# Optimization experiments

Hardware: AMD Instinct MI355X
Metric: run time of the kernel (lower is better)

## Reference

```python
import jax, jax.numpy as jnp
import numpy as np

NEG_SLOPE = 0.2


def gat_conv(x, src, dst, W, att_src, att_dst, bias, heads, out_ch):
    # x: [N, Fin]; src/dst: [E] (self-loops already included)
    N = x.shape[0]
    h = (x @ W).reshape(N, heads, out_ch)                      # [N, H, C]
    a_s = jnp.einsum('nhc,hc->nh', h, att_src)                 # [N, H]
    a_d = jnp.einsum('nhc,hc->nh', h, att_dst)                 # [N, H]
    e = jax.nn.leaky_relu(a_s[src] + a_d[dst], NEG_SLOPE)      # [E, H]
    # segment softmax over incoming edges of each dst node
    e_max = jax.ops.segment_max(e, dst, num_segments=N)        # [N, H]
    p = jnp.exp(e - e_max[dst])                                # [E, H]
    denom = jax.ops.segment_sum(p, dst, num_segments=N)        # [N, H]
    alpha = p / denom[dst]                                     # [E, H]
    msg = h[src] * alpha[:, :, None]                           # [E, H, C]
    out = jax.ops.segment_sum(msg, dst, num_segments=N)        # [N, H, C]
    return out.reshape(N, heads * out_ch) + bias


def setup_inputs() -> dict:
    key = jax.random.key(0)
    ks = jax.random.split(key, 10)
    N, E, F_IN, HID, HEADS, NCLS = 100000, 3200000, 512, 8, 8, 16
    x = jax.random.normal(ks[0], (N, F_IN), dtype=jnp.float32)
    edge_index = jax.random.randint(ks[1], (2, E), 0, N, dtype=jnp.int64)
    s = 1.0 / np.sqrt(F_IN)
    W1 = jax.random.uniform(ks[2], (F_IN, HEADS * HID), jnp.float32, -s, s)
    att_src1 = jax.random.normal(ks[3], (HEADS, HID), jnp.float32) * 0.1
    att_dst1 = jax.random.normal(ks[4], (HEADS, HID), jnp.float32) * 0.1
    b1 = jnp.zeros((HEADS * HID,), jnp.float32)
    s2 = 1.0 / np.sqrt(HEADS * HID)
    W2 = jax.random.uniform(ks[5], (HEADS * HID, NCLS), jnp.float32, -s2, s2)
    att_src2 = jax.random.normal(ks[6], (1, NCLS), jnp.float32) * 0.1
    att_dst2 = jax.random.normal(ks[7], (1, NCLS), jnp.float32) * 0.1
    b2 = jnp.zeros((NCLS,), jnp.float32)
    return {"x": x, "edge_index": edge_index, "W1": W1, "att_src1": att_src1,
            "att_dst1": att_dst1, "b1": b1, "W2": W2, "att_src2": att_src2,
            "att_dst2": att_dst2, "b2": b2}


def reference(x, edge_index, W1, att_src1, att_dst1, b1, W2, att_src2, att_dst2, b2):
    N = x.shape[0]
    loops = jnp.arange(N, dtype=edge_index.dtype)
    src = jnp.concatenate([edge_index[0], loops])  # PyG add_self_loops=True
    dst = jnp.concatenate([edge_index[1], loops])
    # eval mode: F.dropout is identity
    h = gat_conv(x, src, dst, W1, att_src1, att_dst1, b1, heads=8, out_ch=8)
    h = jax.nn.elu(h)
    out = gat_conv(h, src, dst, W2, att_src2, att_dst2, b2, heads=1, out_ch=16)
    return out
```

## Files before the change

### kernel.cpp

```cpp
#include <hip/hip_runtime.h>

#define F_IN 512
#define F1 64
#define NCLS 16
#define NEG_SLOPE 0.2f

typedef __attribute__((ext_vector_type(8))) short short8;
typedef __attribute__((ext_vector_type(4))) float f32x4;

__device__ __forceinline__ unsigned short f2bf(float f) {
    unsigned u = __float_as_uint(f);
    return (unsigned short)((u + 0x7fffu + ((u >> 16) & 1u)) >> 16);
}
__device__ __forceinline__ float bf2f(unsigned short u) {
    return __uint_as_float(((unsigned)u) << 16);
}


__global__ __launch_bounds__(64) void k_detect(const int* __restrict__ ei, int E,
                                               unsigned* __restrict__ mode) {
    int t = threadIdx.x;
    unsigned nz = 0;
    int lim = (E > 256) ? 256 : E;
    for (int k = t; k < lim; k += 64) nz |= (unsigned)ei[2 * k + 1];
    for (int off = 1; off < 64; off <<= 1) nz |= __shfl_xor(nz, off);
    if (t == 0) *mode = (nz == 0) ? 1u : 0u;
}

__device__ __forceinline__ void decode_edge(const int* __restrict__ ei,
                                            const long long* __restrict__ e64,
                                            bool m64, unsigned i, int E, int N,
                                            int& s, int& v) {
    if (i < (unsigned)E) {
        if (m64) { s = (int)e64[i]; v = (int)e64[E + i]; }
        else     { s = ei[i];       v = ei[E + i]; }
    } else {
        s = (int)(i - (unsigned)E);
        v = s;
    }
    s = s < 0 ? 0 : (s >= N ? N - 1 : s);
    v = v < 0 ? 0 : (v >= N ? N - 1 : v);
}

__device__ __forceinline__ int decode_dst(const int* __restrict__ ei,
                                          const long long* __restrict__ e64,
                                          bool m64, unsigned i, int E, int N) {
    int v;
    if (i < (unsigned)E) v = m64 ? (int)e64[E + i] : ei[E + i];
    else                 v = (int)(i - (unsigned)E);
    return v < 0 ? 0 : (v >= N ? N - 1 : v);
}


__global__ __launch_bounds__(256) void k_prep(const float* __restrict__ W1,
                                              unsigned short* __restrict__ W1T) {
    int t = blockIdx.x * 256 + threadIdx.x;
    if (t < F_IN * F1) {
        int k = t >> 6, c = t & 63;
        W1T[(size_t)c * F_IN + k] = f2bf(W1[t]);
    }
}


__device__ __forceinline__ void gemm1_tile(const float* __restrict__ x,
                                           const unsigned short* __restrict__ W1T,
                                           const float* __restrict__ att_s,
                                           const float* __restrict__ att_d,
                                           unsigned short* __restrict__ h1b,
                                           float* __restrict__ a_s1,
                                           float* __restrict__ a_d1,
                                           int N, int row0,
                                           unsigned short (*Abuf)[40],
                                           unsigned short (*BbufT)[40]) {
    const int tid = threadIdx.x;
    const int w = tid >> 6, lane = tid & 63;
    const int quad = lane >> 4, r16 = lane & 15;

    f32x4 acc[4];
#pragma unroll
    for (int t = 0; t < 4; t++) acc[t] = (f32x4){0.f, 0.f, 0.f, 0.f};

    const int a_row = tid >> 2;
    const int a_seg = (tid & 3) * 8;
    const int b_col = tid & 63;
    const int b_kq  = tid >> 6;
    const int ar = row0 + a_row;

    for (int k0 = 0; k0 < F_IN; k0 += 32) {
        {
            float4 v0 = make_float4(0.f, 0.f, 0.f, 0.f), v1 = v0;
            if (ar < N) {
                const float* xp = x + (size_t)ar * F_IN + k0 + a_seg;
                v0 = *(const float4*)xp;
                v1 = *(const float4*)(xp + 4);
            }
            short8 cv;
            cv[0] = (short)f2bf(v0.x); cv[1] = (short)f2bf(v0.y);
            cv[2] = (short)f2bf(v0.z); cv[3] = (short)f2bf(v0.w);
            cv[4] = (short)f2bf(v1.x); cv[5] = (short)f2bf(v1.y);
            cv[6] = (short)f2bf(v1.z); cv[7] = (short)f2bf(v1.w);
            *(short8*)&Abuf[a_row][a_seg] = cv;
        }
        {
            const unsigned short* wp = W1T + (size_t)b_col * F_IN + k0 + b_kq * 8;
            *(short8*)&BbufT[b_col][b_kq * 8] = *(const short8*)wp;
        }
        __syncthreads();

        short8 af = *(const short8*)&Abuf[w * 16 + r16][quad * 8];
#pragma unroll
        for (int t = 0; t < 4; t++) {
            short8 bf = *(const short8*)&BbufT[t * 16 + r16][quad * 8];
            acc[t] = __builtin_amdgcn_mfma_f32_16x16x32_bf16(af, bf, acc[t], 0, 0, 0);
        }
        __syncthreads();
    }

    float ats[4], atd[4];
#pragma unroll
    for (int t = 0; t < 4; t++) {
        ats[t] = att_s[t * 16 + r16];
        atd[t] = att_d[t * 16 + r16];
    }
#pragma unroll
    for (int r = 0; r < 4; r++) {
        int grow = row0 + w * 16 + quad * 4 + r;
        bool ok = grow < N;
        float ps[4], pd[4];
#pragma unroll
        for (int t = 0; t < 4; t++) {
            float vv = acc[t][r];
            if (ok) h1b[(size_t)grow * F1 + t * 16 + r16] = f2bf(vv);
            ps[t] = vv * ats[t];
            pd[t] = vv * atd[t];
        }
#pragma unroll
        for (int t = 0; t < 4; t++) {
            ps[t] += __shfl_xor(ps[t], 1); pd[t] += __shfl_xor(pd[t], 1);
            ps[t] += __shfl_xor(ps[t], 2); pd[t] += __shfl_xor(pd[t], 2);
            ps[t] += __shfl_xor(ps[t], 4); pd[t] += __shfl_xor(pd[t], 4);
        }
        if (ok && (r16 & 7) == 0) {
            int hh0 = r16 >> 3;
#pragma unroll
            for (int t = 0; t < 4; t++) {
                a_s1[(size_t)grow * 8 + t * 2 + hh0] = ps[t];
                a_d1[(size_t)grow * 8 + t * 2 + hh0] = pd[t];
            }
        }
    }
}


__global__ __launch_bounds__(256) void k_fusedA(const float* __restrict__ x,
                                                const unsigned short* __restrict__ W1T,
                                                const float* __restrict__ att_s,
                                                const float* __restrict__ att_d,
                                                unsigned short* __restrict__ h1b,
                                                float* __restrict__ a_s1,
                                                float* __restrict__ a_d1, int N,
                                                const int* __restrict__ ei,
                                                const unsigned* __restrict__ mode,
                                                unsigned* __restrict__ bucketCnt,
                                                int E, int ET, int nch,
                                                int nb, int shift) {
    __shared__ __align__(16) char smem[10240];
    unsigned b = blockIdx.x;
    if ((b & 1) == 0) {
        gemm1_tile(x, W1T, att_s, att_d, h1b, a_s1, a_d1, N, (int)(b >> 1) * 64,
                   (unsigned short (*)[40])smem,
                   (unsigned short (*)[40])(smem + 5120));
        return;
    }
    unsigned* cntL = (unsigned*)smem;
    for (int i = threadIdx.x; i < 1024; i += 256) cntL[i] = 0u;
    __syncthreads();

    const unsigned stride = (unsigned)nch * 256u;
    bool m64 = (*mode != 0u);
    const long long* e64 = (const long long*)ei;
    unsigned i = (b >> 1) * 256u + threadIdx.x;
    for (; i + 3u * stride < (unsigned)ET; i += 4u * stride) {
        int v0 = decode_dst(ei, e64, m64, i, E, N);
        int v1 = decode_dst(ei, e64, m64, i + stride, E, N);
        int v2 = decode_dst(ei, e64, m64, i + 2u * stride, E, N);
        int v3 = decode_dst(ei, e64, m64, i + 3u * stride, E, N);
        atomicAdd(&cntL[(unsigned)v0 >> shift], 1u);
        atomicAdd(&cntL[(unsigned)v1 >> shift], 1u);
        atomicAdd(&cntL[(unsigned)v2 >> shift], 1u);
        atomicAdd(&cntL[(unsigned)v3 >> shift], 1u);
    }
    for (; i < (unsigned)ET; i += stride) {
        int v = decode_dst(ei, e64, m64, i, E, N);
        atomicAdd(&cntL[(unsigned)v >> shift], 1u);
    }
    __syncthreads();
    for (int k = threadIdx.x; k < nb; k += 256) {
        unsigned c = cntL[k];
        if (c) atomicAdd(&bucketCnt[k], c);
    }
}


__global__ __launch_bounds__(256) void k_fusedB(const float* __restrict__ x,
                                                const unsigned short* __restrict__ W1T,
                                                const float* __restrict__ att_s,
                                                const float* __restrict__ att_d,
                                                unsigned short* __restrict__ h1b,
                                                float* __restrict__ a_s1,
                                                float* __restrict__ a_d1, int N,
                                                int rowSplit,
                                                const int* __restrict__ ei,
                                                const unsigned* __restrict__ mode,
                                                unsigned* __restrict__ bucketFill,
                                                unsigned* __restrict__ pairs,
                                                int E, int ET, int nch,
                                                int nb, int shift) {
    __shared__ __align__(16) char smem[10240];
    unsigned b = blockIdx.x;
    if (b & 1) {
        gemm1_tile(x, W1T, att_s, att_d, h1b, a_s1, a_d1, N,
                   rowSplit + (int)(b >> 1) * 64,
                   (unsigned short (*)[40])smem,
                   (unsigned short (*)[40])(smem + 5120));
        return;
    }
    unsigned* cntA = (unsigned*)smem;
    unsigned* ofsA = (unsigned*)(smem + 4096);
    unsigned* part = (unsigned*)(smem + 8192);
    const int t = threadIdx.x;
    const int chunk = (ET + nch - 1) / nch;
    const int cbase = (int)(b >> 1) * chunk;
    const int cend = (cbase + chunk < ET) ? cbase + chunk : ET;
    const unsigned lmask = (1u << shift) - 1u;
    bool m64 = (*mode != 0u);
    const long long* e64 = (const long long*)ei;

    for (int k = t; k < 1024; k += 256) cntA[k] = 0u;
    __syncthreads();
    for (int k = cbase + t; k < cend; k += 256) {
        int v = decode_dst(ei, e64, m64, (unsigned)k, E, N);
        atomicAdd(&cntA[(unsigned)v >> shift], 1u);
    }
    __syncthreads();
    unsigned a0 = cntA[4 * t + 0], a1 = cntA[4 * t + 1];
    unsigned a2 = cntA[4 * t + 2], a3 = cntA[4 * t + 3];
    unsigned ssum = a0 + a1 + a2 + a3;
    part[t] = ssum;
    __syncthreads();
    for (int off = 1; off < 256; off <<= 1) {
        unsigned add = (t >= off) ? part[t - off] : 0u;
        __syncthreads();
        part[t] += add;
        __syncthreads();
    }
    unsigned excl = part[t] - ssum;
    ofsA[4 * t + 0] = excl;
    ofsA[4 * t + 1] = excl + a0;
    ofsA[4 * t + 2] = excl + a0 + a1;
    ofsA[4 * t + 3] = excl + a0 + a1 + a2;
    __syncthreads();
    for (int k = t; k < nb; k += 256) {
        unsigned c = cntA[k];
        unsigned g = c ? atomicAdd(&bucketFill[k], c) : 0u;
        cntA[k] = g - ofsA[k];
    }
    __syncthreads();
    for (int k = cbase + t; k < cend; k += 256) {
        int s, v;
        decode_edge(ei, e64, m64, (unsigned)k, E, N, s, v);
        unsigned bb = (unsigned)v >> shift;
        unsigned slot = atomicAdd(&ofsA[bb], 1u);
        pairs[cntA[bb] + slot] = (unsigned)s | (((unsigned)v & lmask) << 20);
    }
}


__global__ __launch_bounds__(1024) void k_scan_buckets(const unsigned* __restrict__ bucketCnt,
                                                       int nb, int ET,
                                                       unsigned* __restrict__ bucketOfs,
                                                       unsigned* __restrict__ bucketFill,
                                                       unsigned* __restrict__ row_ptr,
                                                       int N) {
    __shared__ unsigned sbuf[1024];
    int t = threadIdx.x;
    unsigned val = (t < nb) ? bucketCnt[t] : 0u;
    sbuf[t] = val;
    __syncthreads();
    for (int off = 1; off < 1024; off <<= 1) {
        unsigned add = (t >= off) ? sbuf[t - off] : 0u;
        __syncthreads();
        sbuf[t] += add;
        __syncthreads();
    }
    if (t < nb) {
        unsigned e = sbuf[t] - val;
        bucketOfs[t] = e;
        bucketFill[t] = e;
    }
    if (t == 0) row_ptr[N] = (unsigned)ET;
}


__global__ __launch_bounds__(256) void k_sort(const unsigned* __restrict__ pairs,
                                              const unsigned* __restrict__ bucketOfs,
                                              const unsigned* __restrict__ bucketCnt,
                                              unsigned* __restrict__ row_ptr,
                                              unsigned* __restrict__ ssrc,
                                              int N, int shift) {
    __shared__ unsigned f[1024];
    __shared__ unsigned part[256];
    const int b = blockIdx.x;
    const int t = threadIdx.x;
    const int nodes = 1 << shift;
    const int bbase = b << shift;
    for (int i = t; i < 1024; i += 256) f[i] = 0u;
    __syncthreads();
    const unsigned base = bucketOfs[b];
    const unsigned cnt = bucketCnt[b];
    for (unsigned i = (unsigned)t; i < cnt; i += 256u)
        atomicAdd(&f[pairs[base + i] >> 20], 1u);
    __syncthreads();
    unsigned a0 = f[4 * t + 0], a1 = f[4 * t + 1];
    unsigned a2 = f[4 * t + 2], a3 = f[4 * t + 3];
    unsigned ssum = a0 + a1 + a2 + a3;
    part[t] = ssum;
    __syncthreads();
    for (int off = 1; off < 256; off <<= 1) {
        unsigned add = (t >= off) ? part[t - off] : 0u;
        __syncthreads();
        part[t] += add;
        __syncthreads();
    }
    unsigned excl = part[t] - ssum;
    unsigned c0 = base + excl;
    unsigned c1 = c0 + a0;
    unsigned c2 = c1 + a1;
    unsigned c3 = c2 + a2;
    {
        int v0 = bbase + 4 * t;
        if (v0 + 0 < N && 4 * t + 0 < nodes) row_ptr[v0 + 0] = c0;
        if (v0 + 1 < N && 4 * t + 1 < nodes) row_ptr[v0 + 1] = c1;
        if (v0 + 2 < N && 4 * t + 2 < nodes) row_ptr[v0 + 2] = c2;
        if (v0 + 3 < N && 4 * t + 3 < nodes) row_ptr[v0 + 3] = c3;
    }
    f[4 * t + 0] = c0;
    f[4 * t + 1] = c1;
    f[4 * t + 2] = c2;
    f[4 * t + 3] = c3;
    __syncthreads();
    for (unsigned i = (unsigned)t; i < cnt; i += 256u) {
        unsigned pk = pairs[base + i];
        unsigned local = pk >> 20;
        unsigned pos = atomicAdd(&f[local], 1u);
        ssrc[pos] = pk & 0xFFFFFu;
    }
}


__global__ __launch_bounds__(256) void k_agg1(const unsigned short* __restrict__ h1b,
                                              const float* __restrict__ a_s1,
                                              const float* __restrict__ a_d1,
                                              const float* __restrict__ b1,
                                              const unsigned* __restrict__ row_ptr,
                                              const unsigned* __restrict__ ssrc,
                                              float* __restrict__ g, int N) {
    int wid = threadIdx.x >> 6, lane = threadIdx.x & 63;
    int v = blockIdx.x * 4 + wid;
    if (v >= N) return;
    unsigned base = row_ptr[v];
    unsigned deg = row_ptr[v + 1] - base;

    const int eA = lane >> 3, hA = lane & 7;
    float adv = a_d1[(size_t)v * 8 + hA];
    const int half = lane >> 5, j32 = lane & 31;
    const int hq = j32 >> 2;

    float denom = 0.f, acc0 = 0.f, acc1 = 0.f;
    for (unsigned jj = 0; jj < deg; jj += 8) {
        unsigned ee = jj + (unsigned)eA;
        bool val = ee < deg;
        unsigned sL = ssrc[base + (val ? ee : 0u)];
        float as = a_s1[(size_t)sL * 8 + hA];
        float eatt = as + adv;
        eatt = eatt > 0.f ? eatt : NEG_SLOPE * eatt;
        float p = val ? __expf(eatt) : 0.f;
        denom += p;
#pragma unroll
        for (int k = 0; k < 4; k++) {
            int esel = k * 2 + half;
            unsigned s_my = (unsigned)__shfl((int)sL, esel * 8);
            float p_my = __shfl(p, esel * 8 + hq);
            unsigned u = *(const unsigned*)(h1b + ((size_t)s_my << 6) + (j32 << 1));
            float lo = __uint_as_float(u << 16);
            float hi = __uint_as_float(u & 0xffff0000u);
            acc0 = fmaf(lo, p_my, acc0);
            acc1 = fmaf(hi, p_my, acc1);
        }
    }
    acc0 += __shfl_xor(acc0, 32);
    acc1 += __shfl_xor(acc1, 32);
    denom += __shfl_xor(denom, 8);
    denom += __shfl_xor(denom, 16);
    denom += __shfl_xor(denom, 32);
    float dn = __shfl(denom, hq);
    if (half == 0) {
        float inv = 1.0f / dn;
        int c0 = j32 * 2;
        float t0 = acc0 * inv + b1[c0];
        float t1 = acc1 * inv + b1[c0 + 1];
        t0 = t0 > 0.f ? t0 : (__expf(t0) - 1.f);
        t1 = t1 > 0.f ? t1 : (__expf(t1) - 1.f);
        *(float2*)&g[(size_t)v * F1 + c0] = make_float2(t0, t1);
    }
}


__global__ __launch_bounds__(256) void k_gemm2(const float* __restrict__ g,
                                               const float* __restrict__ W2,
                                               const float* __restrict__ as2w,
                                               const float* __restrict__ ad2w,
                                               float* __restrict__ h2,
                                               float* __restrict__ a_s2,
                                               float* __restrict__ a_d2, int N) {
    __shared__ float W2s[F1][NCLS];
    int tid = threadIdx.x;
    for (int i = tid; i < F1 * NCLS; i += 256) ((float*)W2s)[i] = W2[i];
    __syncthreads();
    int lane = tid & 63, wid = tid >> 6;
    int n = blockIdx.x * 16 + wid * 4 + (lane >> 4);
    int c = lane & 15;
    if (n >= N) return;
    float acc = 0.f;
#pragma unroll
    for (int k4 = 0; k4 < 16; k4++) {
        float4 gv = *(const float4*)(g + (size_t)n * F1 + k4 * 4);
        acc = fmaf(gv.x, W2s[k4 * 4 + 0][c], acc);
        acc = fmaf(gv.y, W2s[k4 * 4 + 1][c], acc);
        acc = fmaf(gv.z, W2s[k4 * 4 + 2][c], acc);
        acc = fmaf(gv.w, W2s[k4 * 4 + 3][c], acc);
    }
    h2[(size_t)n * NCLS + c] = acc;
    float s = acc * as2w[c];
    float d = acc * ad2w[c];
    s += __shfl_xor(s, 1); s += __shfl_xor(s, 2); s += __shfl_xor(s, 4); s += __shfl_xor(s, 8);
    d += __shfl_xor(d, 1); d += __shfl_xor(d, 2); d += __shfl_xor(d, 4); d += __shfl_xor(d, 8);
    if (c == 0) { a_s2[n] = s; a_d2[n] = d; }
}


__global__ __launch_bounds__(256) void k_agg2(const float* __restrict__ h2,
                                              const float* __restrict__ a_s2,
                                              const float* __restrict__ a_d2,
                                              const float* __restrict__ b2,
                                              const unsigned* __restrict__ row_ptr,
                                              const unsigned* __restrict__ ssrc,
                                              float* __restrict__ out, int N) {
    int wid = threadIdx.x >> 6, lane = threadIdx.x & 63;
    int v = blockIdx.x * 4 + wid;
    if (v >= N) return;
    unsigned base = row_ptr[v];
    unsigned deg = row_ptr[v + 1] - base;
    float adv = a_d2[v];
    int sub = lane >> 4, c = lane & 15;

    float denom = 0.f, acc = 0.f;
    unsigned j = sub;
    for (; j + 12 < deg; j += 16) {
        unsigned s0 = ssrc[base + j + 0];
        unsigned s1 = ssrc[base + j + 4];
        unsigned s2 = ssrc[base + j + 8];
        unsigned s3 = ssrc[base + j + 12];
        float as0 = a_s2[s0];
        float as1 = a_s2[s1];
        float as2 = a_s2[s2];
        float as3 = a_s2[s3];
        float h0 = h2[(size_t)s0 * NCLS + c];
        float h1v = h2[(size_t)s1 * NCLS + c];
        float h2v = h2[(size_t)s2 * NCLS + c];
        float h3 = h2[(size_t)s3 * NCLS + c];
        float e0 = as0 + adv; e0 = e0 > 0.f ? e0 : NEG_SLOPE * e0; float p0 = __expf(e0);
        float e1 = as1 + adv; e1 = e1 > 0.f ? e1 : NEG_SLOPE * e1; float p1 = __expf(e1);
        float e2 = as2 + adv; e2 = e2 > 0.f ? e2 : NEG_SLOPE * e2; float p2 = __expf(e2);
        float e3 = as3 + adv; e3 = e3 > 0.f ? e3 : NEG_SLOPE * e3; float p3 = __expf(e3);
        denom += (p0 + p1) + (p2 + p3);
        acc = fmaf(h0, p0, acc);
        acc = fmaf(h1v, p1, acc);
        acc = fmaf(h2v, p2, acc);
        acc = fmaf(h3, p3, acc);
    }
    for (; j < deg; j += 4) {
        unsigned s = ssrc[base + j];
        float as = a_s2[s];
        float hv = h2[(size_t)s * NCLS + c];
        float e = as + adv; e = e > 0.f ? e : NEG_SLOPE * e;
        float p = __expf(e);
        denom += p;
        acc = fmaf(hv, p, acc);
    }
    acc += __shfl_xor(acc, 16);
    acc += __shfl_xor(acc, 32);
    denom += __shfl_xor(denom, 16);
    denom += __shfl_xor(denom, 32);
    if (lane < 16) {
        out[(size_t)v * NCLS + c] = acc * (1.0f / denom) + b2[c];
    }
}


static inline size_t algn(size_t x) { return (x + 255) & ~(size_t)255; }

extern "C" void kernel_launch(void* const* d_in, const int* in_sizes, int n_in,
                              void* d_out, int out_size, void* d_ws, size_t ws_size,
                              hipStream_t stream) {
    const float* x   = (const float*)d_in[0];
    const int* ei    = (const int*)d_in[1];
    const float* W1  = (const float*)d_in[2];
    const float* as1 = (const float*)d_in[3];
    const float* ad1 = (const float*)d_in[4];
    const float* b1  = (const float*)d_in[5];
    const float* W2  = (const float*)d_in[6];
    const float* as2 = (const float*)d_in[7];
    const float* ad2 = (const float*)d_in[8];
    const float* b2  = (const float*)d_in[9];

    const int N = in_sizes[0] / F_IN;
    const int E = in_sizes[1] / 2;
    const int ET = E + N;

    int shift = 8;
    int nb = (N + 255) >> 8;
    while (nb > 1024) { shift++; nb = (N + (1 << shift) - 1) >> shift; }

    const int GA_T = ((N / 2) + 63) / 64;
    const int rowSplit = GA_T * 64;
    const int GB_T = (N - rowSplit + 63) / 64;

    char* p = (char*)d_ws;
    unsigned short* h1b = (unsigned short*)p;  p += algn((size_t)N * F1 * 2);
    float* g    = (float*)p;      p += algn((size_t)N * F1 * 4);
    float* a_s1 = (float*)p;      p += algn((size_t)N * 8 * 4);
    float* a_d1 = (float*)p;      p += algn((size_t)N * 8 * 4);
    float* h2   = (float*)p;      p += algn((size_t)N * NCLS * 4);
    float* a_s2 = (float*)p;      p += algn((size_t)N * 4);
    float* a_d2 = (float*)p;      p += algn((size_t)N * 4);
    unsigned* row_ptr = (unsigned*)p;  p += algn((size_t)(N + 1) * 4);
    unsigned* bucketCnt  = (unsigned*)p;  p += algn((size_t)1024 * 4);
    unsigned* bucketOfs  = (unsigned*)p;  p += algn((size_t)1024 * 4);
    unsigned* bucketFill = (unsigned*)p;  p += algn((size_t)1024 * 4);
    unsigned* mode    = (unsigned*)p;  p += algn(256);
    unsigned short* W1T = (unsigned short*)p;  p += algn((size_t)F_IN * F1 * 2);
    unsigned* ssrc = (unsigned*)p;     p += algn((size_t)ET * 4);
    unsigned* pairs = (unsigned*)g;

    hipMemsetAsync(bucketCnt, 0, (size_t)nb * 4, stream);

    dim3 b256(256);
    k_detect<<<dim3(1), dim3(64), 0, stream>>>(ei, E, mode);
    k_prep<<<dim3((F_IN * F1 + 255) / 256), b256, 0, stream>>>(W1, W1T);

    k_fusedA<<<dim3(2 * GA_T), b256, 0, stream>>>(x, W1T, as1, ad1, h1b, a_s1, a_d1, N,
                                                  ei, mode, bucketCnt,
                                                  E, ET, GA_T, nb, shift);

    k_scan_buckets<<<dim3(1), dim3(1024), 0, stream>>>(bucketCnt, nb, ET, bucketOfs,
                                                       bucketFill, row_ptr, N);

    k_fusedB<<<dim3(2 * GB_T), b256, 0, stream>>>(x, W1T, as1, ad1, h1b, a_s1, a_d1, N,
                                                  rowSplit, ei, mode, bucketFill,
                                                  pairs, E, ET, GB_T, nb, shift);

    k_sort<<<dim3(nb), b256, 0, stream>>>(pairs, bucketOfs, bucketCnt, row_ptr, ssrc, N, shift);

    k_agg1<<<dim3((N + 3) / 4), b256, 0, stream>>>(h1b, a_s1, a_d1, b1, row_ptr, ssrc, g, N);
    k_gemm2<<<dim3((N + 15) / 16), b256, 0, stream>>>(g, W2, as2, ad2, h2, a_s2, a_d2, N);
    k_agg2<<<dim3((N + 3) / 4), b256, 0, stream>>>(h2, a_s2, a_d2, b2, row_ptr, ssrc,
                                                   (float*)d_out, N);
}
```

Measured before the change: 631.7 us.

## Double-buffer GEMM1 LDS tiles and store gathered a_s1/h2 in fp16

The layer-1 GEMM tile loop now prefetches the next K-slice of x and W1T into registers while MFMAs run on the current LDS buffer. It alternates between two LDS buffers, so each iteration needs one barrier instead of two. Separately, the per-node source attention scores a_s1 and the layer-2 features h2 are stored as fp16, which halves the bytes gathered per edge in the aggregation kernels. The cost is double the shared memory in the fused kernels, which can lower occupancy, plus some precision loss in the attention logits and layer-2 features.

```diff
diff --git a/kernel.cpp b/kernel.cpp
--- a/kernel.cpp
+++ b/kernel.cpp
@@ -1,4 +1,5 @@
 #include <hip/hip_runtime.h>
+#include <hip/hip_fp16.h>
 
 #define F_IN 512
 #define F1 64
@@ -67,11 +68,9 @@
                                            const float* __restrict__ att_s,
                                            const float* __restrict__ att_d,
                                            unsigned short* __restrict__ h1b,
-                                           float* __restrict__ a_s1,
+                                           __half* __restrict__ a_s1,
                                            float* __restrict__ a_d1,
-                                           int N, int row0,
-                                           unsigned short (*Abuf)[40],
-                                           unsigned short (*BbufT)[40]) {
+                                           int N, int row0, char* sm) {
     const int tid = threadIdx.x;
     const int w = tid >> 6, lane = tid & 63;
     const int quad = lane >> 4, r16 = lane & 15;
@@ -85,35 +84,61 @@
     const int b_col = tid & 63;
     const int b_kq  = tid >> 6;
     const int ar = row0 + a_row;
-
-    for (int k0 = 0; k0 < F_IN; k0 += 32) {
+    const bool arok = ar < N;
+    const float* xrow = x + (size_t)ar * F_IN + a_seg;
+    const unsigned short* wrow = W1T + (size_t)b_col * F_IN + b_kq * 8;
+
+    float4 v0 = make_float4(0.f, 0.f, 0.f, 0.f), v1 = v0;
+    short8 rb;
+    if (arok) { v0 = *(const float4*)(xrow); v1 = *(const float4*)(xrow + 4); }
+    rb = *(const short8*)(wrow);
+    {
+        unsigned short (*A)[40] = (unsigned short (*)[40])(sm);
+        unsigned short (*B)[40] = (unsigned short (*)[40])(sm + 5120);
+        short8 cv;
+        cv[0] = (short)f2bf(v0.x); cv[1] = (short)f2bf(v0.y);
+        cv[2] = (short)f2bf(v0.z); cv[3] = (short)f2bf(v0.w);
+        cv[4] = (short)f2bf(v1.x); cv[5] = (short)f2bf(v1.y);
+        cv[6] = (short)f2bf(v1.z); cv[7] = (short)f2bf(v1.w);
+        *(short8*)&A[a_row][a_seg] = cv;
+        *(short8*)&B[b_col][b_kq * 8] = rb;
+    }
+    __syncthreads();
+
+    int cur = 0;
+#pragma unroll
+    for (int k = 0; k < F_IN / 32; k++) {
+        if (k + 1 < F_IN / 32) {
+            v0 = make_float4(0.f, 0.f, 0.f, 0.f); v1 = v0;
+            if (arok) {
+                const float* xp = xrow + (k + 1) * 32;
+                v0 = *(const float4*)xp; v1 = *(const float4*)(xp + 4);
+            }
+            rb = *(const short8*)(wrow + (k + 1) * 32);
+        }
         {
-            float4 v0 = make_float4(0.f, 0.f, 0.f, 0.f), v1 = v0;
-            if (ar < N) {
-                const float* xp = x + (size_t)ar * F_IN + k0 + a_seg;
-                v0 = *(const float4*)xp;
-                v1 = *(const float4*)(xp + 4);
+            unsigned short (*A)[40] = (unsigned short (*)[40])(sm + cur * 10240);
+            unsigned short (*B)[40] = (unsigned short (*)[40])(sm + cur * 10240 + 5120);
+            short8 af = *(const short8*)&A[w * 16 + r16][quad * 8];
+#pragma unroll
+            for (int t = 0; t < 4; t++) {
+                short8 bf = *(const short8*)&B[t * 16 + r16][quad * 8];
+                acc[t] = __builtin_amdgcn_mfma_f32_16x16x32_bf16(af, bf, acc[t], 0, 0, 0);
             }
+        }
+        if (k + 1 < F_IN / 32) {
+            unsigned short (*A)[40] = (unsigned short (*)[40])(sm + (cur ^ 1) * 10240);
+            unsigned short (*B)[40] = (unsigned short (*)[40])(sm + (cur ^ 1) * 10240 + 5120);
             short8 cv;
             cv[0] = (short)f2bf(v0.x); cv[1] = (short)f2bf(v0.y);
             cv[2] = (short)f2bf(v0.z); cv[3] = (short)f2bf(v0.w);
             cv[4] = (short)f2bf(v1.x); cv[5] = (short)f2bf(v1.y);
             cv[6] = (short)f2bf(v1.z); cv[7] = (short)f2bf(v1.w);
-            *(short8*)&Abuf[a_row][a_seg] = cv;
-        }
-        {
-            const unsigned short* wp = W1T + (size_t)b_col * F_IN + k0 + b_kq * 8;
-            *(short8*)&BbufT[b_col][b_kq * 8] = *(const short8*)wp;
+            *(short8*)&A[a_row][a_seg] = cv;
+            *(short8*)&B[b_col][b_kq * 8] = rb;
         }
         __syncthreads();
-
-        short8 af = *(const short8*)&Abuf[w * 16 + r16][quad * 8];
-#pragma unroll
-        for (int t = 0; t < 4; t++) {
-            short8 bf = *(const short8*)&BbufT[t * 16 + r16][quad * 8];
-            acc[t] = __builtin_amdgcn_mfma_f32_16x16x32_bf16(af, bf, acc[t], 0, 0, 0);
-        }
-        __syncthreads();
+        cur ^= 1;
     }
 
     float ats[4], atd[4];
@@ -144,7 +169,7 @@
             int hh0 = r16 >> 3;
 #pragma unroll
             for (int t = 0; t < 4; t++) {
-                a_s1[(size_t)grow * 8 + t * 2 + hh0] = ps[t];
+                a_s1[(size_t)grow * 8 + t * 2 + hh0] = __float2half_rn(ps[t]);
                 a_d1[(size_t)grow * 8 + t * 2 + hh0] = pd[t];
             }
         }
@@ -157,19 +182,17 @@
                                                 const float* __restrict__ att_s,
                                                 const float* __restrict__ att_d,
                                                 unsigned short* __restrict__ h1b,
-                                                float* __restrict__ a_s1,
+                                                __half* __restrict__ a_s1,
                                                 float* __restrict__ a_d1, int N,
                                                 const int* __restrict__ ei,
                                                 const unsigned* __restrict__ mode,
                                                 unsigned* __restrict__ bucketCnt,
                                                 int E, int ET, int nch,
                                                 int nb, int shift) {
-    __shared__ __align__(16) char smem[10240];
+    __shared__ __align__(16) char smem[20480];
     unsigned b = blockIdx.x;
     if ((b & 1) == 0) {
-        gemm1_tile(x, W1T, att_s, att_d, h1b, a_s1, a_d1, N, (int)(b >> 1) * 64,
-                   (unsigned short (*)[40])smem,
-                   (unsigned short (*)[40])(smem + 5120));
+        gemm1_tile(x, W1T, att_s, att_d, h1b, a_s1, a_d1, N, (int)(b >> 1) * 64, smem);
         return;
     }
     unsigned* cntL = (unsigned*)smem;
@@ -207,7 +230,7 @@
                                                 const float* __restrict__ att_s,
                                                 const float* __restrict__ att_d,
                                                 unsigned short* __restrict__ h1b,
-                                                float* __restrict__ a_s1,
+                                                __half* __restrict__ a_s1,
                                                 float* __restrict__ a_d1, int N,
                                                 int rowSplit,
                                                 const int* __restrict__ ei,
@@ -216,13 +239,11 @@
                                                 unsigned* __restrict__ pairs,
                                                 int E, int ET, int nch,
                                                 int nb, int shift) {
-    __shared__ __align__(16) char smem[10240];
+    __shared__ __align__(16) char smem[20480];
     unsigned b = blockIdx.x;
     if (b & 1) {
         gemm1_tile(x, W1T, att_s, att_d, h1b, a_s1, a_d1, N,
-                   rowSplit + (int)(b >> 1) * 64,
-                   (unsigned short (*)[40])smem,
-                   (unsigned short (*)[40])(smem + 5120));
+                   rowSplit + (int)(b >> 1) * 64, smem);
         return;
     }
     unsigned* cntA = (unsigned*)smem;
@@ -359,7 +380,7 @@
 
 
 __global__ __launch_bounds__(256) void k_agg1(const unsigned short* __restrict__ h1b,
-                                              const float* __restrict__ a_s1,
+                                              const __half* __restrict__ a_s1,
                                               const float* __restrict__ a_d1,
                                               const float* __restrict__ b1,
                                               const unsigned* __restrict__ row_ptr,
@@ -381,7 +402,7 @@
         unsigned ee = jj + (unsigned)eA;
         bool val = ee < deg;
         unsigned sL = ssrc[base + (val ? ee : 0u)];
-        float as = a_s1[(size_t)sL * 8 + hA];
+        float as = __half2float(a_s1[(size_t)sL * 8 + hA]);
         float eatt = as + adv;
         eatt = eatt > 0.f ? eatt : NEG_SLOPE * eatt;
         float p = val ? __expf(eatt) : 0.f;
@@ -420,7 +441,7 @@
                                                const float* __restrict__ W2,
                                                const float* __restrict__ as2w,
                                                const float* __restrict__ ad2w,
-                                               float* __restrict__ h2,
+                                               __half* __restrict__ h2,
                                                float* __restrict__ a_s2,
                                                float* __restrict__ a_d2, int N) {
     __shared__ float W2s[F1][NCLS];
@@ -440,7 +461,7 @@
         acc = fmaf(gv.z, W2s[k4 * 4 + 2][c], acc);
         acc = fmaf(gv.w, W2s[k4 * 4 + 3][c], acc);
     }
-    h2[(size_t)n * NCLS + c] = acc;
+    h2[(size_t)n * NCLS + c] = __float2half_rn(acc);
     float s = acc * as2w[c];
     float d = acc * ad2w[c];
     s += __shfl_xor(s, 1); s += __shfl_xor(s, 2); s += __shfl_xor(s, 4); s += __shfl_xor(s, 8);
@@ -449,7 +470,7 @@
 }
 
 
-__global__ __launch_bounds__(256) void k_agg2(const float* __restrict__ h2,
+__global__ __launch_bounds__(256) void k_agg2(const __half* __restrict__ h2,
                                               const float* __restrict__ a_s2,
                                               const float* __restrict__ a_d2,
                                               const float* __restrict__ b2,
@@ -475,10 +496,10 @@
         float as1 = a_s2[s1];
         float as2 = a_s2[s2];
         float as3 = a_s2[s3];
-        float h0 = h2[(size_t)s0 * NCLS + c];
-        float h1v = h2[(size_t)s1 * NCLS + c];
-        float h2v = h2[(size_t)s2 * NCLS + c];
-        float h3 = h2[(size_t)s3 * NCLS + c];
+        float h0 = __half2float(h2[(size_t)s0 * NCLS + c]);
+        float h1v = __half2float(h2[(size_t)s1 * NCLS + c]);
+        float h2v = __half2float(h2[(size_t)s2 * NCLS + c]);
+        float h3 = __half2float(h2[(size_t)s3 * NCLS + c]);
         float e0 = as0 + adv; e0 = e0 > 0.f ? e0 : NEG_SLOPE * e0; float p0 = __expf(e0);
         float e1 = as1 + adv; e1 = e1 > 0.f ? e1 : NEG_SLOPE * e1; float p1 = __expf(e1);
         float e2 = as2 + adv; e2 = e2 > 0.f ? e2 : NEG_SLOPE * e2; float p2 = __expf(e2);
@@ -492,7 +513,7 @@
     for (; j < deg; j += 4) {
         unsigned s = ssrc[base + j];
         float as = a_s2[s];
-        float hv = h2[(size_t)s * NCLS + c];
+        float hv = __half2float(h2[(size_t)s * NCLS + c]);
         float e = as + adv; e = e > 0.f ? e : NEG_SLOPE * e;
         float p = __expf(e);
         denom += p;
@@ -539,9 +560,9 @@
     char* p = (char*)d_ws;
     unsigned short* h1b = (unsigned short*)p;  p += algn((size_t)N * F1 * 2);
     float* g    = (float*)p;      p += algn((size_t)N * F1 * 4);
-    float* a_s1 = (float*)p;      p += algn((size_t)N * 8 * 4);
+    __half* a_s1 = (__half*)p;    p += algn((size_t)N * 8 * 2);
     float* a_d1 = (float*)p;      p += algn((size_t)N * 8 * 4);
-    float* h2   = (float*)p;      p += algn((size_t)N * NCLS * 4);
+    __half* h2  = (__half*)p;     p += algn((size_t)N * NCLS * 2);
     float* a_s2 = (float*)p;      p += algn((size_t)N * 4);
     float* a_d2 = (float*)p;      p += algn((size_t)N * 4);
     unsigned* row_ptr = (unsigned*)p;  p += algn((size_t)(N + 1) * 4);
```

After: 596.7 us. 1.06x faster.
